# Kernel optimization log

Hardware: AMD Instinct MI355X
Metric: run time of the kernel (lower is better)

Reference implementation:

```python
import jax, jax.numpy as jnp
import numpy as np

N_HEADS = 4
ITERS = 3
EPS = 1e-8


def layer_norm(x, g, b, eps=1e-5):
    m = jnp.mean(x, axis=-1, keepdims=True)
    v = jnp.mean((x - m) ** 2, axis=-1, keepdims=True)
    return (x - m) * jax.lax.rsqrt(v + eps) * g + b


def gru_cell(x, h, Wih, Whh, bih, bhh):
    # PyTorch GRUCell semantics. x: [M, kvq], h: [M, dim]
    gi = x @ Wih.T + bih
    gh = h @ Whh.T + bhh
    ir, iz, i_n = jnp.split(gi, 3, axis=-1)
    hr, hz, h_n = jnp.split(gh, 3, axis=-1)
    r = jax.nn.sigmoid(ir + hr)
    z = jax.nn.sigmoid(iz + hz)
    n = jnp.tanh(i_n + r * h_n)
    return (1.0 - z) * n + z * h


def slot_attention(features, slots, Wq, Wk, Wv, g_in, b_in, g_s, b_s, Wih, Whh, bih, bhh):
    b, n, _ = features.shape
    _, ns, dim = slots.shape
    kvq = Wk.shape[0]
    dh = kvq // N_HEADS
    scale = dh ** -0.5
    inp = layer_norm(features, g_in, b_in)
    k = (inp @ Wk.T).reshape(b, n, N_HEADS, dh)
    v = (inp @ Wv.T).reshape(b, n, N_HEADS, dh)
    attn_vis = None
    for _ in range(ITERS):
        slots_prev = slots
        s = layer_norm(slots, g_s, b_s)
        q = (s @ Wq.T).reshape(b, ns, N_HEADS, dh)
        dots = jnp.einsum("bihd,bjhd->bihj", q, k) * scale
        attn = jax.nn.softmax(dots, axis=1)  # competitive softmax over slots
        attn_vis = attn.mean(axis=2)  # [b, ns, n]
        w = attn + EPS
        w = w / jnp.sum(w, axis=-1, keepdims=True)  # weighted mean over features
        upd = jnp.einsum("bjhd,bihj->bihd", v, w).reshape(b, ns, kvq)
        slots = gru_cell(upd.reshape(-1, kvq), slots_prev.reshape(-1, dim),
                         Wih, Whh, bih, bhh).reshape(b, ns, dim)
    return slots, attn_vis


def vq_pool(x, codebook):
    # x: [b, ns, d], codebook: [C, d]
    d2 = (jnp.sum(x ** 2, axis=-1, keepdims=True)
          - 2.0 * jnp.einsum("bnd,cd->bnc", x, codebook)
          + jnp.sum(codebook ** 2, axis=-1))
    idx = jnp.argmin(d2, axis=-1)
    q = codebook[idx]
    commit = jnp.mean((x - jax.lax.stop_gradient(q)) ** 2)
    q = x + jax.lax.stop_gradient(q - x)  # straight-through
    return q, idx, commit


def setup_inputs() -> dict:
    key = jax.random.key(0)
    ks = jax.random.split(key, 16)
    B, N, FD = 32, 1024, 768
    NS, D, KVQ, C = 24, 256, 256, 512
    sc = lambda d: d ** -0.5
    return {
        "features": jax.random.normal(ks[0], (B, N, FD), jnp.float32),
        "conditioning": jax.random.normal(ks[1], (B, NS, D), jnp.float32),
        "Wq": jax.random.normal(ks[2], (KVQ, D), jnp.float32) * sc(D),
        "Wk": jax.random.normal(ks[3], (KVQ, FD), jnp.float32) * sc(FD),
        "Wv": jax.random.normal(ks[4], (KVQ, FD), jnp.float32) * sc(FD),
        "g_in": jnp.ones((FD,), jnp.float32),
        "b_in": jnp.zeros((FD,), jnp.float32),
        "g_s": jnp.ones((D,), jnp.float32),
        "b_s": jnp.zeros((D,), jnp.float32),
        "Wih": jax.random.normal(ks[5], (3 * D, KVQ), jnp.float32) * sc(KVQ),
        "Whh": jax.random.normal(ks[6], (3 * D, D), jnp.float32) * sc(D),
        "bih": jnp.zeros((3 * D,), jnp.float32),
        "bhh": jnp.zeros((3 * D,), jnp.float32),
        "codebook": jax.random.normal(ks[7], (C, D), jnp.float32) * sc(D),
    }


def reference(features, conditioning, Wq, Wk, Wv, g_in, b_in, g_s, b_s,
              Wih, Whh, bih, bhh, codebook):
    sa = lambda f, s: slot_attention(f, s, Wq, Wk, Wv, g_in, b_in, g_s, b_s,
                                     Wih, Whh, bih, bhh)
    slots, pre_attn = sa(features, conditioning)
    q_slots, indices, commit = vq_pool(slots, codebook)
    slots, post_attn = sa(features, q_slots)
    return slots, post_attn, pre_attn, indices, commit
```

## Files before the change

### kernel.cpp

```cpp
#include <hip/hip_runtime.h>
#include <math.h>

#define LB __launch_bounds__(256)

constexpr int BATCH = 32, NFEAT = 1024, FDIM = 768, NSLOT = 24;
constexpr int NH = 4, DH = 64, NITER = 3;
constexpr int MF = BATCH * NFEAT;
constexpr int MS = BATCH * NSLOT;
constexpr float QSCALE = 0.125f;
constexpr float ATTN_EPS = 1e-8f;
constexpr float LNEPS = 1e-5f;

typedef __attribute__((ext_vector_type(8))) short bf16x8;
typedef __attribute__((ext_vector_type(4))) float f32x4;

__device__ __forceinline__ unsigned short f2bf(float x) {
  unsigned u = __float_as_uint(x);
  return (unsigned short)((u + 0x7FFFu + ((u >> 16) & 1u)) >> 16);
}
__device__ __forceinline__ float bf2f(unsigned short h) {
  return __uint_as_float(((unsigned)h) << 16);
}
__device__ __forceinline__ void cvt8(const float4& a, const float4& b, float m, float r,
                                     int4& hi, int4& lo) {
  float v[8] = {a.x, a.y, a.z, a.w, b.x, b.y, b.z, b.w};
  unsigned sh[8], sl[8];
#pragma unroll
  for (int j = 0; j < 8; ++j) {
    float vv = (v[j] - m) * r;
    unsigned short h = f2bf(vv);
    sh[j] = h;
    sl[j] = f2bf(vv - bf2f(h));
  }
  hi = make_int4((int)(sh[0] | (sh[1] << 16)), (int)(sh[2] | (sh[3] << 16)),
                 (int)(sh[4] | (sh[5] << 16)), (int)(sh[6] | (sh[7] << 16)));
  lo = make_int4((int)(sl[0] | (sl[1] << 16)), (int)(sl[2] | (sl[3] << 16)),
                 (int)(sl[4] | (sl[5] << 16)), (int)(sl[6] | (sl[7] << 16)));
}

__device__ __forceinline__ void gll16(const void* g, void* l) {
  __builtin_amdgcn_global_load_lds(
      (const __attribute__((address_space(1))) void*)g,
      (__attribute__((address_space(3))) void*)l, 16, 0, 0);
}

__global__ LB void k_preprow(const float* __restrict__ x, float* __restrict__ stats,
                             const float* __restrict__ Wk, const float* __restrict__ Wv,
                             const float* __restrict__ Wq,
                             const float* __restrict__ g_in, const float* __restrict__ b_in,
                             const float* __restrict__ g_s, const float* __restrict__ b_s,
                             short* __restrict__ Bh_g, short* __restrict__ Bl_g,
                             short* __restrict__ Wgqh, short* __restrict__ Wgql,
                             float* __restrict__ cconst) {
  const int t = threadIdx.x;
  if (blockIdx.x < MF / 4) {
    const int row = blockIdx.x * 4 + (t >> 6);
    const int lane = t & 63;
    const float* xr = x + (size_t)row * FDIM;
    float s = 0.f, sq = 0.f;
#pragma unroll
    for (int i = 0; i < 3; ++i) {
      float4 v = *(const float4*)(xr + i * 256 + lane * 4);
      s += v.x + v.y + v.z + v.w;
      sq += v.x * v.x + v.y * v.y + v.z * v.z + v.w * v.w;
    }
#pragma unroll
    for (int o = 32; o > 0; o >>= 1) { s += __shfl_down(s, o, 64); sq += __shfl_down(sq, o, 64); }
    if (lane == 0) {
      float m = s / (float)FDIM;
      float var = sq / (float)FDIM - m * m;
      stats[row * 2] = m;
      stats[row * 2 + 1] = 1.f / sqrtf(var + LNEPS);
    }
    return;
  }
  const int r = blockIdx.x - MF / 4;
  float s = 0.f;
  if (r < 512) {
    const float* srcW = (r < 256) ? (Wk + (size_t)r * FDIM) : (Wv + (size_t)(r - 256) * FDIM);
    for (int k = t; k < FDIM; k += 256) {
      float w = srcW[k];
      float wg = w * g_in[k];
      s += b_in[k] * w;
      unsigned short h = f2bf(wg);
      Bh_g[(size_t)r * FDIM + k] = (short)h;
      Bl_g[(size_t)r * FDIM + k] = (short)f2bf(wg - bf2f(h));
    }
  } else {
    const int c = r - 512;
    float w = Wq[(size_t)c * 256 + t];
    float wg = w * g_s[t];
    unsigned short hh = f2bf(wg);
    Wgqh[(size_t)c * 256 + t] = (short)hh;
    Wgql[(size_t)c * 256 + t] = (short)f2bf(wg - bf2f(hh));
    s = b_s[t] * w;
  }
  __shared__ float red[256];
  red[t] = s; __syncthreads();
  for (int o = 128; o > 0; o >>= 1) { if (t < o) red[t] += red[t + o]; __syncthreads(); }
  if (t == 0) cconst[r] = red[0];
}

union SmemM {
  struct { short Ah[2048], Al[2048], Bh[2][4096], Bl[2][4096]; } m;
  struct { short vh[128][72], vl[128][72]; } e;
};

__global__ LB void k_mfkv(const float* __restrict__ x, const float* __restrict__ stats,
                          const short* __restrict__ Bh_g, const short* __restrict__ Bl_g,
                          const float* __restrict__ cconst,
                          short* __restrict__ khi, short* __restrict__ klo,
                          short* __restrict__ vThi, short* __restrict__ vTlo) {
  __shared__ SmemM sm;
  const int t = threadIdx.x;
  const int l = t & 63;
  const int w = t >> 6;
  const int row0 = blockIdx.x * 64;
  const int c0 = blockIdx.y * 128;

  const int sAr = t >> 2;
  const int sl = t & 3;
  const int kqA = sl ^ ((sAr >> 1) & 3);
  const float* pa = x + (size_t)(row0 + sAr) * FDIM + kqA * 8;
  const float mA = stats[(row0 + sAr) * 2], rA = stats[(row0 + sAr) * 2 + 1];
  const int sBr1 = sAr + 64;
  const int kqB1 = sl ^ ((sBr1 >> 1) & 3);
  const short* pkh0 = Bh_g + (size_t)(c0 + sAr) * FDIM + kqA * 8;
  const short* pkh1 = Bh_g + (size_t)(c0 + sBr1) * FDIM + kqB1 * 8;
  const short* pkl0 = Bl_g + (size_t)(c0 + sAr) * FDIM + kqA * 8;
  const short* pkl1 = Bl_g + (size_t)(c0 + sBr1) * FDIM + kqB1 * 8;
  const short* pvh0 = Bh_g + (size_t)(256 + c0 + sAr) * FDIM + kqA * 8;
  const short* pvh1 = Bh_g + (size_t)(256 + c0 + sBr1) * FDIM + kqB1 * 8;
  const short* pvl0 = Bl_g + (size_t)(256 + c0 + sAr) * FDIM + kqA * 8;
  const short* pvl1 = Bl_g + (size_t)(256 + c0 + sBr1) * FDIM + kqB1 * 8;
  const int wbA = t * 16;
  const int wb0 = t * 16, wb1 = (t + 256) * 16;

  const int wm = (w >> 1) * 32, wn = (w & 1) * 64;
  int aoff[2], boff[4];
#pragma unroll
  for (int m = 0; m < 2; ++m) {
    const int ar = wm + m * 16 + (l & 15);
    const int kq = l >> 4;
    aoff[m] = ar * 64 + ((kq ^ ((ar >> 1) & 3)) << 4);
  }
#pragma unroll
  for (int n = 0; n < 4; ++n) {
    const int bc = wn + n * 16 + (l & 15);
    const int kq = l >> 4;
    boff[n] = bc * 64 + ((kq ^ ((bc >> 1) & 3)) << 4);
  }

  f32x4 acc[2][2][4] = {};
  float4 raa = *(const float4*)pa, rab = *(const float4*)(pa + 4);

  for (int s = 0; s < FDIM / 32; ++s) {
    if (s) __syncthreads();
    const int ko = s * 32;
    gll16(pkh0 + ko, (char*)&sm.m.Bh[0][0] + wb0);
    gll16(pkh1 + ko, (char*)&sm.m.Bh[0][0] + wb1);
    gll16(pkl0 + ko, (char*)&sm.m.Bl[0][0] + wb0);
    gll16(pkl1 + ko, (char*)&sm.m.Bl[0][0] + wb1);
    gll16(pvh0 + ko, (char*)&sm.m.Bh[1][0] + wb0);
    gll16(pvh1 + ko, (char*)&sm.m.Bh[1][0] + wb1);
    gll16(pvl0 + ko, (char*)&sm.m.Bl[1][0] + wb0);
    gll16(pvl1 + ko, (char*)&sm.m.Bl[1][0] + wb1);
    int4 hi, lo;
    cvt8(raa, rab, mA, rA, hi, lo);
    *(int4*)((char*)sm.m.Ah + wbA) = hi; *(int4*)((char*)sm.m.Al + wbA) = lo;
    if (s + 1 < FDIM / 32) {
      raa = *(const float4*)(pa + ko + 32);
      rab = *(const float4*)(pa + ko + 36);
    }
    __syncthreads();
    bf16x8 fah[2], fal[2];
#pragma unroll
    for (int m = 0; m < 2; ++m) {
      fah[m] = *(const bf16x8*)((const char*)sm.m.Ah + aoff[m]);
      fal[m] = *(const bf16x8*)((const char*)sm.m.Al + aoff[m]);
    }
#pragma unroll
    for (int kv = 0; kv < 2; ++kv) {
      bf16x8 fbh[4], fbl[4];
#pragma unroll
      for (int n = 0; n < 4; ++n) {
        fbh[n] = *(const bf16x8*)((const char*)&sm.m.Bh[kv][0] + boff[n]);
        fbl[n] = *(const bf16x8*)((const char*)&sm.m.Bl[kv][0] + boff[n]);
      }
#pragma unroll
      for (int m = 0; m < 2; ++m)
#pragma unroll
        for (int n = 0; n < 4; ++n) {
          acc[kv][m][n] = __builtin_amdgcn_mfma_f32_16x16x32_bf16(fal[m], fbh[n], acc[kv][m][n], 0, 0, 0);
          acc[kv][m][n] = __builtin_amdgcn_mfma_f32_16x16x32_bf16(fah[m], fbl[n], acc[kv][m][n], 0, 0, 0);
          acc[kv][m][n] = __builtin_amdgcn_mfma_f32_16x16x32_bf16(fah[m], fbh[n], acc[kv][m][n], 0, 0, 0);
        }
    }
  }
  __syncthreads();
  const int b_blk = row0 >> 10;
  const int jbase = row0 & 1023;
#pragma unroll
  for (int m = 0; m < 2; ++m) {
    const int rloc = wm + m * 16 + ((l >> 4) << 2);
    const int rbase = row0 + rloc;
#pragma unroll
    for (int n = 0; n < 4; ++n) {
      const int col = wn + n * 16 + (l & 15);
      const int gcol = c0 + col;
      const float cck = cconst[gcol];
      const float ccv = cconst[256 + gcol];
      unsigned vhp[2] = {0, 0}, vlp[2] = {0, 0};
#pragma unroll
      for (int r = 0; r < 4; ++r) {
        const float kval = acc[0][m][n][r] + cck;
        const unsigned short h = f2bf(kval);
        khi[(size_t)(rbase + r) * 256 + gcol] = (short)h;
        klo[(size_t)(rbase + r) * 256 + gcol] = (short)f2bf(kval - bf2f(h));
        const float vval = acc[1][m][n][r] + ccv;
        const unsigned short hv = f2bf(vval);
        const unsigned short lv = f2bf(vval - bf2f(hv));
        vhp[r >> 1] |= ((unsigned)hv) << ((r & 1) * 16);
        vlp[r >> 1] |= ((unsigned)lv) << ((r & 1) * 16);
      }
      *(int2*)((short*)&sm.e.vh[0][0] + col * 72 + rloc) = make_int2((int)vhp[0], (int)vhp[1]);
      *(int2*)((short*)&sm.e.vl[0][0] + col * 72 + rloc) = make_int2((int)vlp[0], (int)vlp[1]);
    }
  }
  __syncthreads();
  {
    const int vr = t >> 1;
    const int vh2 = (t & 1) * 32;
    const int gcol = c0 + vr;
    const int hh2 = gcol >> 6, dh = gcol & 63;
    const size_t vrow = ((size_t)(b_blk * 4 + hh2) * 64 + dh) * 1024 + jbase + vh2;
    const short* sh2 = (const short*)&sm.e.vh[0][0] + vr * 72 + vh2;
    const short* sl2 = (const short*)&sm.e.vl[0][0] + vr * 72 + vh2;
#pragma unroll
    for (int q = 0; q < 4; ++q) {
      *(int4*)(vThi + vrow + q * 8) = *(const int4*)(sh2 + q * 8);
      *(int4*)(vTlo + vrow + q * 8) = *(const int4*)(sl2 + q * 8);
    }
  }
}

template <bool WRITE_ATTN>
__global__ LB void k_fdots(const float* __restrict__ slots,
                           const short* __restrict__ Wgqh, const short* __restrict__ Wgql,
                           const float* __restrict__ cconst,
                           const short* __restrict__ khi, const short* __restrict__ klo,
                           const short* __restrict__ vThi, const short* __restrict__ vTlo,
                           float* __restrict__ attn, float* __restrict__ updp,
                           float* __restrict__ ssump) {
  const int blk = blockIdx.x;
  const int jc = blk & 3;
  const int h = (blk >> 2) & 3;
  const int b = blk >> 4;
  const int t = threadIdx.x;
  const int l = t & 63;
  const int w = t >> 6;
  __shared__ float sc[24 * 256];
  __shared__ short sh_[32 * 256];
  __shared__ short sl_[32 * 256];
  __shared__ short qh[2048], ql[2048];
  __shared__ float part[4][NSLOT];
  __shared__ float mst[NSLOT], rst[NSLOT];

  if (t < 192) {
    const int r = t >> 3, g = t & 7;
    const float* sr = slots + (size_t)(b * NSLOT + r) * 256 + g * 32;
    float s = 0.f, sq = 0.f;
#pragma unroll
    for (int m4 = 0; m4 < 8; ++m4) {
      float4 v = *(const float4*)(sr + m4 * 4);
      *(float4*)&sc[r * 256 + g * 32 + m4 * 4] = v;
      s += v.x + v.y + v.z + v.w;
      sq += v.x * v.x + v.y * v.y + v.z * v.z + v.w * v.w;
    }
    s += __shfl_down(s, 4, 8); sq += __shfl_down(sq, 4, 8);
    s += __shfl_down(s, 2, 8); sq += __shfl_down(sq, 2, 8);
    s += __shfl_down(s, 1, 8); sq += __shfl_down(sq, 1, 8);
    if (g == 0) {
      float mm = s * (1.f / 256.f);
      mst[r] = mm;
      rst[r] = 1.f / sqrtf(sq * (1.f / 256.f) - mm * mm + LNEPS);
    }
  }
  __syncthreads();
#pragma unroll 4
  for (int i = 0; i < NSLOT; ++i) {
    const float v = (sc[i * 256 + t] - mst[i]) * rst[i];
    const unsigned short hh = f2bf(v);
    const int slot = i * 32 + ((t >> 3) ^ (i & 31));
    sh_[slot * 8 + (t & 7)] = (short)hh;
    sl_[slot * 8 + (t & 7)] = (short)f2bf(v - bf2f(hh));
  }
  __syncthreads();
  {
    f32x4 qacc[2] = {};
#pragma unroll
    for (int ks = 0; ks < 8; ++ks) {
      bf16x8 ah[2], al[2];
#pragma unroll
      for (int m = 0; m < 2; ++m) {
        const int row = m * 16 + (l & 15);
        const int g = ks * 4 + (l >> 4);
        const int slot = row * 32 + (g ^ (row & 31));
        ah[m] = *(const bf16x8*)&sh_[slot * 8];
        al[m] = *(const bf16x8*)&sl_[slot * 8];
      }
      const size_t brow = (size_t)(h * 64 + w * 16 + (l & 15)) * 256 + ks * 32 + (l >> 4) * 8;
      const bf16x8 bh = *(const bf16x8*)(Wgqh + brow);
      const bf16x8 bl2 = *(const bf16x8*)(Wgql + brow);
#pragma unroll
      for (int m = 0; m < 2; ++m) {
        qacc[m] = __builtin_amdgcn_mfma_f32_16x16x32_bf16(al[m], bh, qacc[m], 0, 0, 0);
        qacc[m] = __builtin_amdgcn_mfma_f32_16x16x32_bf16(ah[m], bl2, qacc[m], 0, 0, 0);
        qacc[m] = __builtin_amdgcn_mfma_f32_16x16x32_bf16(ah[m], bh, qacc[m], 0, 0, 0);
      }
    }
    const int d = w * 16 + (l & 15);
    const float qc = cconst[512 + h * 64 + d];
#pragma unroll
    for (int m = 0; m < 2; ++m)
#pragma unroll
      for (int r = 0; r < 4; ++r) {
        const int row = m * 16 + (l >> 4) * 4 + r;
        const float qv = qacc[m][r] + qc;
        const unsigned short hh = f2bf(qv);
        const int slot = row * 8 + ((d >> 3) ^ (row & 7));
        qh[slot * 8 + (d & 7)] = (short)hh;
        ql[slot * 8 + (d & 7)] = (short)f2bf(qv - bf2f(hh));
      }
  }
  __syncthreads();
  {
    const short* khb = khi + (size_t)(b * NFEAT + jc * 256) * 256 + h * 64;
    const short* klb = klo + (size_t)(b * NFEAT + jc * 256) * 256 + h * 64;
    f32x4 scc[2][4] = {};
#pragma unroll
    for (int ks = 0; ks < 2; ++ks) {
      bf16x8 ah[2], al[2];
#pragma unroll
      for (int m = 0; m < 2; ++m) {
        const int row = m * 16 + (l & 15);
        const int g = ks * 4 + (l >> 4);
        const int slot = row * 8 + (g ^ (row & 7));
        ah[m] = *(const bf16x8*)&qh[slot * 8];
        al[m] = *(const bf16x8*)&ql[slot * 8];
      }
#pragma unroll
      for (int nl = 0; nl < 4; ++nl) {
        const int nt = w * 4 + nl;
        const size_t boffg = (size_t)(nt * 16 + (l & 15)) * 256 + ks * 32 + (l >> 4) * 8;
        const bf16x8 bh = *(const bf16x8*)(khb + boffg);
        const bf16x8 bl2 = *(const bf16x8*)(klb + boffg);
#pragma unroll
        for (int m = 0; m < 2; ++m) {
          scc[m][nl] = __builtin_amdgcn_mfma_f32_16x16x32_bf16(al[m], bh, scc[m][nl], 0, 0, 0);
          scc[m][nl] = __builtin_amdgcn_mfma_f32_16x16x32_bf16(ah[m], bl2, scc[m][nl], 0, 0, 0);
          scc[m][nl] = __builtin_amdgcn_mfma_f32_16x16x32_bf16(ah[m], bh, scc[m][nl], 0, 0, 0);
        }
      }
    }
#pragma unroll
    for (int m = 0; m < 2; ++m)
#pragma unroll
      for (int nl = 0; nl < 4; ++nl) {
        const int col = (w * 4 + nl) * 16 + (l & 15);
        const int rbase = m * 16 + ((l >> 4) << 2);
#pragma unroll
        for (int r = 0; r < 4; ++r)
          if (rbase + r < 24) sc[(rbase + r) * 256 + col] = scc[m][nl][r];
      }
  }
  __syncthreads();
  {
    float acc[NSLOT];
#pragma unroll
    for (int i = 0; i < NSLOT; ++i) acc[i] = sc[i * 256 + t];
    float mx = -1e30f;
#pragma unroll
    for (int i = 0; i < NSLOT; ++i) { acc[i] *= QSCALE; mx = fmaxf(mx, acc[i]); }
    float s = 0.f;
#pragma unroll
    for (int i = 0; i < NSLOT; ++i) { acc[i] = expf(acc[i] - mx); s += acc[i]; }
    const float inv = 1.f / s;
    float* ab = attn + (size_t)(b * NH + h) * NSLOT * NFEAT + jc * 256 + t;
#pragma unroll
    for (int i = 0; i < NSLOT; ++i) {
      const float wgt = acc[i] * inv;
      if (WRITE_ATTN) ab[(size_t)i * NFEAT] = wgt;
      const float ae = wgt + ATTN_EPS;
      acc[i] = ae;
      const unsigned short hh = f2bf(ae);
      const int slot = i * 32 + ((t >> 3) ^ (i & 31));
      sh_[slot * 8 + (t & 7)] = (short)hh;
      sl_[slot * 8 + (t & 7)] = (short)f2bf(ae - bf2f(hh));
    }
#pragma unroll
    for (int i = 0; i < NSLOT; ++i) {
      float rs = acc[i];
#pragma unroll
      for (int o = 32; o > 0; o >>= 1) rs += __shfl_down(rs, o, 64);
      if (l == 0) part[w][i] = rs;
    }
  }
  __syncthreads();
  {
    f32x4 pacc[2] = {};
#pragma unroll
    for (int ks = 0; ks < 8; ++ks) {
      bf16x8 ah[2], al[2];
#pragma unroll
      for (int m = 0; m < 2; ++m) {
        const int row = m * 16 + (l & 15);
        const int g = ks * 4 + (l >> 4);
        const int slot = row * 32 + (g ^ (row & 31));
        ah[m] = *(const bf16x8*)&sh_[slot * 8];
        al[m] = *(const bf16x8*)&sl_[slot * 8];
      }
      const size_t brow = ((size_t)(b * 4 + h) * 64 + w * 16 + (l & 15)) * 1024 +
                          jc * 256 + ks * 32 + (l >> 4) * 8;
      const bf16x8 bh = *(const bf16x8*)(vThi + brow);
      const bf16x8 bl2 = *(const bf16x8*)(vTlo + brow);
#pragma unroll
      for (int m = 0; m < 2; ++m) {
        pacc[m] = __builtin_amdgcn_mfma_f32_16x16x32_bf16(al[m], bh, pacc[m], 0, 0, 0);
        pacc[m] = __builtin_amdgcn_mfma_f32_16x16x32_bf16(ah[m], bl2, pacc[m], 0, 0, 0);
        pacc[m] = __builtin_amdgcn_mfma_f32_16x16x32_bf16(ah[m], bh, pacc[m], 0, 0, 0);
      }
    }
    const int d = w * 16 + (l & 15);
    float* up = updp + (size_t)((b * 4 + h) * 4 + jc) * NSLOT * 64;
#pragma unroll
    for (int m = 0; m < 2; ++m)
#pragma unroll
      for (int r = 0; r < 4; ++r) {
        const int row = m * 16 + (l >> 4) * 4 + r;
        if (row < 24) up[row * 64 + d] = pacc[m][r];
      }
  }
  if (t < NSLOT)
    ssump[((size_t)(b * 4 + h) * 4 + jc) * NSLOT + t] =
        part[0][t] + part[1][t] + part[2][t] + part[3][t];
}

template <bool FINAL>
__global__ LB void k_grufin(const float* __restrict__ updp, const float* __restrict__ ssump,
                            const float* __restrict__ sprev,
                            const float* __restrict__ Wih, const float* __restrict__ Whh,
                            const float* __restrict__ bih, const float* __restrict__ bhh,
                            float* __restrict__ snext, float* __restrict__ outs,
                            const float* __restrict__ attn, float* __restrict__ vis_out) {
  __shared__ float updt[8][256];
  __shared__ float Bs[3][64][33];
  const int bx = blockIdx.x;
  const int d0 = blockIdx.y * 32;
  const int rows0 = bx * 8;
  const int t = threadIdx.x;
  {
    const int h = t >> 6, d = t & 63;
#pragma unroll
    for (int u = 0; u < 8; ++u) {
      const int row = rows0 + u;
      const int b = row / 24, i = row - b * 24;
      const size_t base = (size_t)(b * 4 + h) * 4;
      float s = 0.f, wsum = 0.f;
#pragma unroll
      for (int jc = 0; jc < 4; ++jc) {
        s += updp[(base + jc) * (NSLOT * 64) + i * 64 + d];
        wsum += ssump[(base + jc) * NSLOT + i];
      }
      updt[u][h * 64 + d] = s / wsum;
    }
  }
  __syncthreads();
  const int r = t >> 5;
  const int dd = t & 31;
  float accR = 0.f, accZ = 0.f, accN = 0.f, accH = 0.f;
  for (int k0 = 0; k0 < 256; k0 += 64) {
#pragma unroll
    for (int ii = 0; ii < 6; ++ii) {
      const int i = ii * 256 + t;
      const int s = i / 512, rem = i & 511, c = rem >> 4, kq = rem & 15;
      float4 wv = *(const float4*)(Wih + (size_t)(s * 256 + d0 + c) * 256 + k0 + kq * 4);
      Bs[s][kq * 4 + 0][c] = wv.x; Bs[s][kq * 4 + 1][c] = wv.y;
      Bs[s][kq * 4 + 2][c] = wv.z; Bs[s][kq * 4 + 3][c] = wv.w;
    }
    __syncthreads();
#pragma unroll
    for (int kk = 0; kk < 64; ++kk) {
      const float a = updt[r][k0 + kk];
      accR += a * Bs[0][kk][dd];
      accZ += a * Bs[1][kk][dd];
      accN += a * Bs[2][kk][dd];
    }
    __syncthreads();
  }
  {
    const int rr2 = t >> 5, c0 = (t & 31) * 8;
    const float* sp = sprev + (size_t)(rows0 + rr2) * 256 + c0;
    *(float4*)&updt[rr2][c0] = *(const float4*)sp;
    *(float4*)&updt[rr2][c0 + 4] = *(const float4*)(sp + 4);
  }
  __syncthreads();
  for (int k0 = 0; k0 < 256; k0 += 64) {
#pragma unroll
    for (int ii = 0; ii < 6; ++ii) {
      const int i = ii * 256 + t;
      const int s = i / 512, rem = i & 511, c = rem >> 4, kq = rem & 15;
      float4 wv = *(const float4*)(Whh + (size_t)(s * 256 + d0 + c) * 256 + k0 + kq * 4);
      Bs[s][kq * 4 + 0][c] = wv.x; Bs[s][kq * 4 + 1][c] = wv.y;
      Bs[s][kq * 4 + 2][c] = wv.z; Bs[s][kq * 4 + 3][c] = wv.w;
    }
    __syncthreads();
#pragma unroll
    for (int kk = 0; kk < 64; ++kk) {
      const float a = updt[r][k0 + kk];
      accR += a * Bs[0][kk][dd];
      accZ += a * Bs[1][kk][dd];
      accH += a * Bs[2][kk][dd];
    }
    __syncthreads();
  }
  const int row = rows0 + r;
  const int c = d0 + dd;
  const float hp = updt[r][c];
  const float rr = 1.f / (1.f + expf(-(accR + bih[c] + bhh[c])));
  const float zz = 1.f / (1.f + expf(-(accZ + bih[256 + c] + bhh[256 + c])));
  const float nn = tanhf(accN + bih[512 + c] + rr * (accH + bhh[512 + c]));
  const float o = (1.f - zz) * nn + zz * hp;
  snext[(size_t)row * 256 + c] = o;
  if (FINAL) {
    outs[(size_t)row * 256 + c] = o;
    const int gid = (blockIdx.y * 96 + blockIdx.x) * 256 + t;
#pragma unroll
    for (int z = 0; z < 4; ++z) {
      const int idx = z * 196608 + gid;
      const int j = idx & 1023;
      const int rem = idx >> 10;
      const int i = rem % NSLOT;
      const int b = rem / NSLOT;
      float s = 0.f;
#pragma unroll
      for (int hh = 0; hh < NH; ++hh)
        s += attn[(size_t)((b * NH + hh) * NSLOT + i) * NFEAT + j];
      vis_out[idx] = 0.25f * s;
    }
  }
}

__global__ LB void k_vqvis(float* __restrict__ slots, const float* __restrict__ cb,
                           const float* __restrict__ attn,
                           float* __restrict__ idx_out, float* __restrict__ bestd2,
                           float* __restrict__ vis_out) {
  const int t = threadIdx.x;
  if (blockIdx.x >= MS) {
    const int idx = (blockIdx.x - MS) * 256 + t;
    const int j = idx & 1023;
    const int rem = idx >> 10;
    const int i = rem % NSLOT;
    const int b = rem / NSLOT;
    float s = 0.f;
#pragma unroll
    for (int h = 0; h < NH; ++h)
      s += attn[(size_t)((b * NH + h) * NSLOT + i) * NFEAT + j];
    vis_out[idx] = 0.25f * s;
    return;
  }
  const int r = blockIdx.x;
  __shared__ float xs[256];
  __shared__ float red[256];
  __shared__ float rv[256];
  __shared__ int ri[256];
  xs[t] = slots[(size_t)r * 256 + t];
  __syncthreads();
  red[t] = xs[t] * xs[t]; __syncthreads();
  for (int o = 128; o > 0; o >>= 1) { if (t < o) red[t] += red[t + o]; __syncthreads(); }
  const float x2 = red[0];
  float best = 1e30f; int bidx = 0;
#pragma unroll
  for (int cset = 0; cset < 2; ++cset) {
    const int c = cset * 256 + t;
    const float* cr = cb + (size_t)c * 256;
    float xc = 0.f, cc = 0.f;
    for (int dd = 0; dd < 256; dd += 4) {
      float4 cv = *(const float4*)(cr + dd);
      xc += xs[dd] * cv.x + xs[dd + 1] * cv.y + xs[dd + 2] * cv.z + xs[dd + 3] * cv.w;
      cc += cv.x * cv.x + cv.y * cv.y + cv.z * cv.z + cv.w * cv.w;
    }
    float d2 = x2 - 2.f * xc + cc;
    if (d2 < best) { best = d2; bidx = c; }
  }
  rv[t] = best; ri[t] = bidx; __syncthreads();
  for (int o = 128; o > 0; o >>= 1) {
    if (t < o) {
      if (rv[t + o] < rv[t] || (rv[t + o] == rv[t] && ri[t + o] < ri[t])) {
        rv[t] = rv[t + o]; ri[t] = ri[t + o];
      }
    }
    __syncthreads();
  }
  const int wi = ri[0];
  const float cval = cb[(size_t)wi * 256 + t];
  const float diff = xs[t] - cval;
  red[t] = diff * diff; __syncthreads();
  for (int o = 128; o > 0; o >>= 1) { if (t < o) red[t] += red[t + o]; __syncthreads(); }
  if (t == 0) { idx_out[r] = (float)wi; bestd2[r] = red[0]; }
  slots[(size_t)r * 256 + t] = cval;
}

__global__ LB void k_commit(const float* __restrict__ bestd2, float* __restrict__ out) {
  const int t = threadIdx.x;
  __shared__ float red[256];
  float s = 0.f;
  for (int i = t; i < MS; i += 256) s += bestd2[i];
  red[t] = s; __syncthreads();
  for (int o = 128; o > 0; o >>= 1) { if (t < o) red[t] += red[t + o]; __syncthreads(); }
  if (t == 0) out[0] = red[0] / (float)(MS * 256);
}

extern "C" void kernel_launch(void* const* d_in, const int* in_sizes, int n_in,
                              void* d_out, int out_size, void* d_ws, size_t ws_size,
                              hipStream_t stream) {
  const float* features = (const float*)d_in[0];
  const float* cond = (const float*)d_in[1];
  const float* Wq = (const float*)d_in[2];
  const float* Wk = (const float*)d_in[3];
  const float* Wv = (const float*)d_in[4];
  const float* g_in = (const float*)d_in[5];
  const float* b_in = (const float*)d_in[6];
  const float* g_s = (const float*)d_in[7];
  const float* b_s = (const float*)d_in[8];
  const float* Wih = (const float*)d_in[9];
  const float* Whh = (const float*)d_in[10];
  const float* bih = (const float*)d_in[11];
  const float* bhh = (const float*)d_in[12];
  const float* cb = (const float*)d_in[13];
  float* out = (float*)d_out;

  char* wsb = (char*)d_ws;
  short* Bh_g = (short*)wsb; wsb += (size_t)512 * FDIM * 2;
  short* Bl_g = (short*)wsb; wsb += (size_t)512 * FDIM * 2;
  short* khi = (short*)wsb; wsb += (size_t)MF * 256 * 2;
  short* klo = (short*)wsb; wsb += (size_t)MF * 256 * 2;
  short* vThi = (short*)wsb; wsb += (size_t)MF * 256 * 2;
  short* vTlo = (short*)wsb; wsb += (size_t)MF * 256 * 2;
  short* Wgqh = (short*)wsb; wsb += (size_t)256 * 256 * 2;
  short* Wgql = (short*)wsb; wsb += (size_t)256 * 256 * 2;
  float* ws = (float*)wsb;
  float* stats = ws;  ws += 2 * MF;
  float* attn = ws;   ws += (size_t)BATCH * NH * NSLOT * NFEAT;
  float* sbufA = ws;  ws += (size_t)MS * 256;
  float* sbufB = ws;  ws += (size_t)MS * 256;
  float* updp = ws;   ws += (size_t)512 * NSLOT * 64;
  float* ssump = ws;  ws += (size_t)512 * NSLOT;
  float* cconst = ws; ws += 768;
  float* bestd2 = ws; ws += MS;

  float* out_slots = out;
  float* out_post = out + 196608;
  float* out_pre = out + 196608 + 786432;
  float* out_idx = out + 196608 + 786432 * 2;
  float* out_commit = out_idx + 768;

  k_preprow<<<MF / 4 + 768, 256, 0, stream>>>(features, stats, Wk, Wv, Wq, g_in, b_in,
                                              g_s, b_s, Bh_g, Bl_g, Wgqh, Wgql, cconst);
  k_mfkv<<<dim3(MF / 64, 2), 256, 0, stream>>>(features, stats, Bh_g, Bl_g, cconst,
                                               khi, klo, vThi, vTlo);

  const float* scur = cond;
  float* bufs[2] = {sbufA, sbufB};
  int nb = 0;
  for (int call = 0; call < 2; ++call) {
    for (int it = 0; it < NITER; ++it) {
      float* snxt = bufs[nb]; nb ^= 1;
      if (it == NITER - 1)
        k_fdots<true><<<512, 256, 0, stream>>>(scur, Wgqh, Wgql, cconst, khi, klo,
                                               vThi, vTlo, attn, updp, ssump);
      else
        k_fdots<false><<<512, 256, 0, stream>>>(scur, Wgqh, Wgql, cconst, khi, klo,
                                                vThi, vTlo, attn, updp, ssump);
      if (call == 1 && it == NITER - 1)
        k_grufin<true><<<dim3(MS / 8, 8), 256, 0, stream>>>(updp, ssump, scur, Wih, Whh,
                                                            bih, bhh, snxt, out_slots,
                                                            attn, out_post);
      else
        k_grufin<false><<<dim3(MS / 8, 8), 256, 0, stream>>>(updp, ssump, scur, Wih, Whh,
                                                             bih, bhh, snxt, out_slots,
                                                             nullptr, nullptr);
      scur = snxt;
    }
    if (call == 0) {
      k_vqvis<<<MS + BATCH * NSLOT * NFEAT / 256, 256, 0, stream>>>(
          (float*)scur, cb, attn, out_idx, bestd2, out_pre);
      k_commit<<<1, 256, 0, stream>>>(bestd2, out_commit);
    }
  }
}
```

Measured before the change: 559.9 us.

## Split fdots feature chunks into eight per head and fuse slot layernorm into registers

The attention kernel now handles 128 features per block instead of 256 and launches 1024 blocks instead of 512. This shrinks the score buffer in shared memory and aims to improve occupancy and latency hiding, though only half the threads take part in the softmax stage. The slot layernorm is now computed in registers using shuffles and vectorized bf16 hi/lo conversion, which removes a shared-memory staging pass and one barrier. The q padding rows are explicitly zeroed. The GRU kernel now reduces eight partial sums per head instead of four, which doubles the partial buffer traffic and the redundant recomputation of the per-block q projection.

```diff
diff --git a/kernel.cpp b/kernel.cpp
--- a/kernel.cpp
+++ b/kernel.cpp
@@ -253,47 +253,46 @@
                            float* __restrict__ attn, float* __restrict__ updp,
                            float* __restrict__ ssump) {
   const int blk = blockIdx.x;
-  const int jc = blk & 3;
-  const int h = (blk >> 2) & 3;
-  const int b = blk >> 4;
+  const int jc = blk & 7;
+  const int h = (blk >> 3) & 3;
+  const int b = blk >> 5;
   const int t = threadIdx.x;
   const int l = t & 63;
   const int w = t >> 6;
-  __shared__ float sc[24 * 256];
   __shared__ short sh_[32 * 256];
   __shared__ short sl_[32 * 256];
+  __shared__ float sc[24 * 128];
   __shared__ short qh[2048], ql[2048];
-  __shared__ float part[4][NSLOT];
-  __shared__ float mst[NSLOT], rst[NSLOT];
+  __shared__ float part[2][NSLOT];
 
   if (t < 192) {
     const int r = t >> 3, g = t & 7;
     const float* sr = slots + (size_t)(b * NSLOT + r) * 256 + g * 32;
+    float4 va[8];
     float s = 0.f, sq = 0.f;
 #pragma unroll
     for (int m4 = 0; m4 < 8; ++m4) {
-      float4 v = *(const float4*)(sr + m4 * 4);
-      *(float4*)&sc[r * 256 + g * 32 + m4 * 4] = v;
-      s += v.x + v.y + v.z + v.w;
-      sq += v.x * v.x + v.y * v.y + v.z * v.z + v.w * v.w;
+      va[m4] = *(const float4*)(sr + m4 * 4);
+      s += va[m4].x + va[m4].y + va[m4].z + va[m4].w;
+      sq += va[m4].x * va[m4].x + va[m4].y * va[m4].y +
+            va[m4].z * va[m4].z + va[m4].w * va[m4].w;
     }
     s += __shfl_down(s, 4, 8); sq += __shfl_down(sq, 4, 8);
     s += __shfl_down(s, 2, 8); sq += __shfl_down(sq, 2, 8);
     s += __shfl_down(s, 1, 8); sq += __shfl_down(sq, 1, 8);
-    if (g == 0) {
-      float mm = s * (1.f / 256.f);
-      mst[r] = mm;
-      rst[r] = 1.f / sqrtf(sq * (1.f / 256.f) - mm * mm + LNEPS);
-    }
-  }
-  __syncthreads();
-#pragma unroll 4
-  for (int i = 0; i < NSLOT; ++i) {
-    const float v = (sc[i * 256 + t] - mst[i]) * rst[i];
-    const unsigned short hh = f2bf(v);
-    const int slot = i * 32 + ((t >> 3) ^ (i & 31));
-    sh_[slot * 8 + (t & 7)] = (short)hh;
-    sl_[slot * 8 + (t & 7)] = (short)f2bf(v - bf2f(hh));
+    const float st = __shfl(s, l & 56, 64);
+    const float sqt = __shfl(sq, l & 56, 64);
+    const float mm = st * (1.f / 256.f);
+    const float rr = 1.f / sqrtf(sqt * (1.f / 256.f) - mm * mm + LNEPS);
+#pragma unroll
+    for (int m4 = 0; m4 < 8; m4 += 2) {
+      int4 hi, lo;
+      cvt8(va[m4], va[m4 + 1], mm, rr, hi, lo);
+      const int gi = g * 4 + (m4 >> 1);
+      const int slot = r * 32 + (gi ^ (r & 31));
+      *(int4*)&sh_[slot * 8] = hi;
+      *(int4*)&sl_[slot * 8] = lo;
+    }
   }
   __syncthreads();
   {
@@ -326,18 +325,28 @@
 #pragma unroll
       for (int r = 0; r < 4; ++r) {
         const int row = m * 16 + (l >> 4) * 4 + r;
-        const float qv = qacc[m][r] + qc;
-        const unsigned short hh = f2bf(qv);
-        const int slot = row * 8 + ((d >> 3) ^ (row & 7));
-        qh[slot * 8 + (d & 7)] = (short)hh;
-        ql[slot * 8 + (d & 7)] = (short)f2bf(qv - bf2f(hh));
-      }
+        if (row < 24) {
+          const float qv = qacc[m][r] + qc;
+          const unsigned short hh = f2bf(qv);
+          const int slot = row * 8 + ((d >> 3) ^ (row & 7));
+          qh[slot * 8 + (d & 7)] = (short)hh;
+          ql[slot * 8 + (d & 7)] = (short)f2bf(qv - bf2f(hh));
+        }
+      }
+  }
+#pragma unroll
+  for (int z = 0; z < 2; ++z) {
+    const int e = z * 256 + t;
+    const int row = 24 + (e >> 6), dd2 = e & 63;
+    const int slot = row * 8 + ((dd2 >> 3) ^ (row & 7));
+    qh[slot * 8 + (dd2 & 7)] = 0;
+    ql[slot * 8 + (dd2 & 7)] = 0;
   }
   __syncthreads();
   {
-    const short* khb = khi + (size_t)(b * NFEAT + jc * 256) * 256 + h * 64;
-    const short* klb = klo + (size_t)(b * NFEAT + jc * 256) * 256 + h * 64;
-    f32x4 scc[2][4] = {};
+    const short* khb = khi + (size_t)(b * NFEAT + jc * 128) * 256 + h * 64;
+    const short* klb = klo + (size_t)(b * NFEAT + jc * 128) * 256 + h * 64;
+    f32x4 scc[2][2] = {};
 #pragma unroll
     for (int ks = 0; ks < 2; ++ks) {
       bf16x8 ah[2], al[2];
@@ -350,8 +359,8 @@
         al[m] = *(const bf16x8*)&ql[slot * 8];
       }
 #pragma unroll
-      for (int nl = 0; nl < 4; ++nl) {
-        const int nt = w * 4 + nl;
+      for (int nl = 0; nl < 2; ++nl) {
+        const int nt = w * 2 + nl;
         const size_t boffg = (size_t)(nt * 16 + (l & 15)) * 256 + ks * 32 + (l >> 4) * 8;
         const bf16x8 bh = *(const bf16x8*)(khb + boffg);
         const bf16x8 bl2 = *(const bf16x8*)(klb + boffg);
@@ -366,19 +375,19 @@
 #pragma unroll
     for (int m = 0; m < 2; ++m)
 #pragma unroll
-      for (int nl = 0; nl < 4; ++nl) {
-        const int col = (w * 4 + nl) * 16 + (l & 15);
+      for (int nl = 0; nl < 2; ++nl) {
+        const int col = (w * 2 + nl) * 16 + (l & 15);
         const int rbase = m * 16 + ((l >> 4) << 2);
 #pragma unroll
         for (int r = 0; r < 4; ++r)
-          if (rbase + r < 24) sc[(rbase + r) * 256 + col] = scc[m][nl][r];
-      }
-  }
-  __syncthreads();
-  {
+          if (rbase + r < 24) sc[(rbase + r) * 128 + col] = scc[m][nl][r];
+      }
+  }
+  __syncthreads();
+  if (t < 128) {
     float acc[NSLOT];
 #pragma unroll
-    for (int i = 0; i < NSLOT; ++i) acc[i] = sc[i * 256 + t];
+    for (int i = 0; i < NSLOT; ++i) acc[i] = sc[i * 128 + t];
     float mx = -1e30f;
 #pragma unroll
     for (int i = 0; i < NSLOT; ++i) { acc[i] *= QSCALE; mx = fmaxf(mx, acc[i]); }
@@ -386,7 +395,7 @@
 #pragma unroll
     for (int i = 0; i < NSLOT; ++i) { acc[i] = expf(acc[i] - mx); s += acc[i]; }
     const float inv = 1.f / s;
-    float* ab = attn + (size_t)(b * NH + h) * NSLOT * NFEAT + jc * 256 + t;
+    float* ab = attn + (size_t)(b * NH + h) * NSLOT * NFEAT + jc * 128 + t;
 #pragma unroll
     for (int i = 0; i < NSLOT; ++i) {
       const float wgt = acc[i] * inv;
@@ -394,7 +403,7 @@
       const float ae = wgt + ATTN_EPS;
       acc[i] = ae;
       const unsigned short hh = f2bf(ae);
-      const int slot = i * 32 + ((t >> 3) ^ (i & 31));
+      const int slot = i * 16 + ((t >> 3) ^ (i & 15));
       sh_[slot * 8 + (t & 7)] = (short)hh;
       sl_[slot * 8 + (t & 7)] = (short)f2bf(ae - bf2f(hh));
     }
@@ -410,18 +419,18 @@
   {
     f32x4 pacc[2] = {};
 #pragma unroll
-    for (int ks = 0; ks < 8; ++ks) {
+    for (int ks = 0; ks < 4; ++ks) {
       bf16x8 ah[2], al[2];
 #pragma unroll
       for (int m = 0; m < 2; ++m) {
         const int row = m * 16 + (l & 15);
         const int g = ks * 4 + (l >> 4);
-        const int slot = row * 32 + (g ^ (row & 31));
+        const int slot = row * 16 + (g ^ (row & 15));
         ah[m] = *(const bf16x8*)&sh_[slot * 8];
         al[m] = *(const bf16x8*)&sl_[slot * 8];
       }
       const size_t brow = ((size_t)(b * 4 + h) * 64 + w * 16 + (l & 15)) * 1024 +
-                          jc * 256 + ks * 32 + (l >> 4) * 8;
+                          jc * 128 + ks * 32 + (l >> 4) * 8;
       const bf16x8 bh = *(const bf16x8*)(vThi + brow);
       const bf16x8 bl2 = *(const bf16x8*)(vTlo + brow);
 #pragma unroll
@@ -432,7 +441,7 @@
       }
     }
     const int d = w * 16 + (l & 15);
-    float* up = updp + (size_t)((b * 4 + h) * 4 + jc) * NSLOT * 64;
+    float* up = updp + (size_t)((b * 4 + h) * 8 + jc) * NSLOT * 64;
 #pragma unroll
     for (int m = 0; m < 2; ++m)
 #pragma unroll
@@ -442,8 +451,7 @@
       }
   }
   if (t < NSLOT)
-    ssump[((size_t)(b * 4 + h) * 4 + jc) * NSLOT + t] =
-        part[0][t] + part[1][t] + part[2][t] + part[3][t];
+    ssump[((size_t)(b * 4 + h) * 8 + jc) * NSLOT + t] = part[0][t] + part[1][t];
 }
 
 template <bool FINAL>
@@ -465,10 +473,10 @@
     for (int u = 0; u < 8; ++u) {
       const int row = rows0 + u;
       const int b = row / 24, i = row - b * 24;
-      const size_t base = (size_t)(b * 4 + h) * 4;
+      const size_t base = (size_t)(b * 4 + h) * 8;
       float s = 0.f, wsum = 0.f;
 #pragma unroll
-      for (int jc = 0; jc < 4; ++jc) {
+      for (int jc = 0; jc < 8; ++jc) {
         s += updp[(base + jc) * (NSLOT * 64) + i * 64 + d];
         wsum += ssump[(base + jc) * NSLOT + i];
       }
@@ -654,8 +662,8 @@
   float* attn = ws;   ws += (size_t)BATCH * NH * NSLOT * NFEAT;
   float* sbufA = ws;  ws += (size_t)MS * 256;
   float* sbufB = ws;  ws += (size_t)MS * 256;
-  float* updp = ws;   ws += (size_t)512 * NSLOT * 64;
-  float* ssump = ws;  ws += (size_t)512 * NSLOT;
+  float* updp = ws;   ws += (size_t)1024 * NSLOT * 64;
+  float* ssump = ws;  ws += (size_t)1024 * NSLOT;
   float* cconst = ws; ws += 768;
   float* bestd2 = ws; ws += MS;
 
@@ -677,11 +685,11 @@
     for (int it = 0; it < NITER; ++it) {
       float* snxt = bufs[nb]; nb ^= 1;
       if (it == NITER - 1)
-        k_fdots<true><<<512, 256, 0, stream>>>(scur, Wgqh, Wgql, cconst, khi, klo,
-                                               vThi, vTlo, attn, updp, ssump);
+        k_fdots<true><<<1024, 256, 0, stream>>>(scur, Wgqh, Wgql, cconst, khi, klo,
+                                                vThi, vTlo, attn, updp, ssump);
       else
-        k_fdots<false><<<512, 256, 0, stream>>>(scur, Wgqh, Wgql, cconst, khi, klo,
-                                                vThi, vTlo, attn, updp, ssump);
+        k_fdots<false><<<1024, 256, 0, stream>>>(scur, Wgqh, Wgql, cconst, khi, klo,
+                                                 vThi, vTlo, attn, updp, ssump);
       if (call == 1 && it == NITER - 1)
         k_grufin<true><<<dim3(MS / 8, 8), 256, 0, stream>>>(updp, ssump, scur, Wih, Whh,
                                                             bih, bhh, snxt, out_slots,
```

Measured after the change: 604.2 us. 7.9% more time.
